# Kernel tuning notes

Measured on AMD Instinct MI355X. Metric: run time of the kernel, lower is better.

Reference implementation:

```python
import jax, jax.numpy as jnp
import numpy as np

B, S, H = 4, 2048, 1024
E, K, F = 8, 2, 4096


def setup_inputs() -> dict:
    key = jax.random.key(0)
    ks = jax.random.split(key, 6)
    x = jax.random.normal(ks[0], (B, S, H), dtype=jnp.float32)
    gate_w = jax.random.normal(ks[1], (H, E), dtype=jnp.float32) * 0.02
    w1 = jax.random.normal(ks[2], (E, H, F), dtype=jnp.float32) * 0.02
    b1 = jnp.zeros((E, F), dtype=jnp.float32)
    w2 = jax.random.normal(ks[3], (E, F, H), dtype=jnp.float32) * 0.02
    b2 = jnp.zeros((E, H), dtype=jnp.float32)
    return {"x": x, "gate_w": gate_w, "w1": w1, "b1": b1, "w2": w2, "b2": b2}


def reference(x, gate_w, w1, b1, w2, b2):
    # NOTE: the torch module masks expert inputs per token, but since each
    # expert's output is re-masked by the same mask, the math is exactly
    # out[t] = sum_i renorm_prob[t,i] * expert_{topk_idx[t,i]}(x[t]).
    # Dropout is identity in eval mode.
    T = B * S
    x_flat = x.reshape(T, H)

    gate_scores = x_flat @ gate_w                      # [T, E]
    gate_probs = jax.nn.softmax(gate_scores, axis=-1)  # [T, E]
    topk_vals, topk_idx = jax.lax.top_k(gate_probs, K)  # [T, K]
    topk_w = jax.nn.softmax(topk_vals, axis=-1)        # renormalize via softmax (as in source)

    # Combine weights per (token, expert): sum over top-k slots.
    onehot = jax.nn.one_hot(topk_idx, E, dtype=x.dtype)           # [T, K, E]
    comb = jnp.einsum('tk,tke->te', topk_w, onehot)               # [T, E]

    # Run all experts densely (faithful to naive module; combine masks out unrouted).
    h = jnp.einsum('th,ehf->etf', x_flat, w1) + b1[:, None, :]    # [E, T, F]
    h = jax.nn.relu(h)
    expert_out = jnp.einsum('etf,efh->eth', h, w2) + b2[:, None, :]  # [E, T, H]

    out_flat = jnp.einsum('te,eth->th', comb, expert_out)         # [T, H]
    output = out_flat.reshape(B, S, H)

    # Load-balance loss: KL(uniform || softmax(mean gate prob)), batchmean over E.
    expert_usage = gate_probs.mean(axis=0)                        # [E]
    log_sm = jax.nn.log_softmax(expert_usage, axis=0)
    uniform = jnp.full((E,), 1.0 / E, dtype=x.dtype)
    kl = jnp.sum(uniform * (jnp.log(uniform) - log_sm)) / E
    load_balance_loss = 0.01 * kl
    return output, load_balance_loss
```

## Files before the change

kernel.cpp:

```cpp
#include <hip/hip_runtime.h>
#include <stdint.h>

#define T_TOK 8192
#define HD 1024
#define NE 8
#define FD 4096
#define RALLOC 18432
#define G1 1152
#define G2 384
#define NKT1 16
#define GATE_BLOCKS 1024

typedef __attribute__((ext_vector_type(8))) short bf16x8;
typedef __attribute__((ext_vector_type(4))) float f32x4;
typedef __attribute__((ext_vector_type(4))) short s16x4;

__device__ __forceinline__ unsigned short f2bf(float f) {
  unsigned u = __builtin_bit_cast(unsigned, f);
  u += 0x7fffu + ((u >> 16) & 1u);
  return (unsigned short)(u >> 16);
}

__device__ __forceinline__ void gld_lds16(const void* g, void* l) {
  __builtin_amdgcn_global_load_lds(
      (const __attribute__((address_space(1))) void*)g,
      (__attribute__((address_space(3))) void*)l, 16, 0, 0);
}

__global__ __launch_bounds__(256) void k_transpose2(const float* __restrict__ w1,
                                                    const float* __restrict__ w2,
                                                    unsigned short* __restrict__ w1t,
                                                    unsigned short* __restrict__ w2t) {
  __shared__ unsigned short tile[64 * 80];
  const int i = blockIdx.x;
  const float* src;
  unsigned short* dst;
  int R, C, r0, c0;
  if (i < 8192) {
    const int e = i >> 10, rem = i & 1023;
    R = HD; C = FD; r0 = (rem >> 6) << 6; c0 = (rem & 63) << 6;
    src = w1 + (size_t)e * R * C; dst = w1t + (size_t)e * R * C;
  } else {
    const int e = (i - 8192) >> 10, rem = (i - 8192) & 1023;
    R = FD; C = HD; r0 = (rem >> 4) << 6; c0 = (rem & 15) << 6;
    src = w2 + (size_t)e * R * C; dst = w2t + (size_t)e * R * C;
  }
  const int tid = threadIdx.x;
  {
    const int r = tid >> 2, cg = (tid & 3) * 16;
    #pragma unroll
    for (int m = 0; m < 4; ++m) {
      float4 v = *(const float4*)(src + (size_t)(r0 + r) * C + c0 + cg + 4 * m);
      s16x4 pv;
      pv[0] = (short)f2bf(v.x); pv[1] = (short)f2bf(v.y);
      pv[2] = (short)f2bf(v.z); pv[3] = (short)f2bf(v.w);
      *(s16x4*)&tile[r * 80 + cg + 4 * m] = pv;
    }
  }
  __syncthreads();
  {
    const int c = tid >> 2, rg = (tid & 3) * 16;
    bf16x8 v0, v1;
    #pragma unroll
    for (int j = 0; j < 8; ++j) v0[j] = (short)tile[(rg + j) * 80 + c];
    #pragma unroll
    for (int j = 0; j < 8; ++j) v1[j] = (short)tile[(rg + 8 + j) * 80 + c];
    unsigned short* dp = dst + (size_t)(c0 + c) * R + r0 + rg;
    *(bf16x8*)dp = v0;
    *(bf16x8*)(dp + 8) = v1;
  }
}

__global__ __launch_bounds__(512) void k_gating(const float* __restrict__ x,
                                                const float* __restrict__ gw,
                                                int* __restrict__ toke,
                                                float* __restrict__ tokw,
                                                int* __restrict__ counts8,
                                                double* __restrict__ part,
                                                unsigned short* __restrict__ xbf) {
  __shared__ float gwT[8 * 1024];
  __shared__ double sp[8][8];
  __shared__ int scnt[8];
  const int tid = threadIdx.x;
  const int lane = tid & 63;
  const int w = tid >> 6;
  if (tid < 8) scnt[tid] = 0;
  #pragma unroll
  for (int rep = 0; rep < 16; ++rep) {
    int idx = rep * 512 + tid;
    gwT[(idx & 7) * 1024 + (idx >> 3)] = gw[idx];
  }
  __syncthreads();

  const int t = blockIdx.x * 8 + w;
  double acc[8];
  #pragma unroll
  for (int e = 0; e < 8; ++e) acc[e] = 0.0;
  const float* xr = x + (size_t)t * HD;
  unsigned short* xbr = xbf + (size_t)t * HD;
  #pragma unroll
  for (int j = 0; j < 4; ++j) {
    const int hh = j * 256 + lane * 4;
    float4 xv = *(const float4*)(xr + hh);
    s16x4 pv;
    pv[0] = (short)f2bf(xv.x); pv[1] = (short)f2bf(xv.y);
    pv[2] = (short)f2bf(xv.z); pv[3] = (short)f2bf(xv.w);
    *(s16x4*)(xbr + hh) = pv;
    #pragma unroll
    for (int e = 0; e < 8; ++e) {
      float4 gv = *(const float4*)(gwT + e * 1024 + hh);
      acc[e] += (double)xv.x * (double)gv.x;
      acc[e] += (double)xv.y * (double)gv.y;
      acc[e] += (double)xv.z * (double)gv.z;
      acc[e] += (double)xv.w * (double)gv.w;
    }
  }
  for (int off = 32; off > 0; off >>= 1) {
    #pragma unroll
    for (int e = 0; e < 8; ++e) acc[e] += __shfl_xor(acc[e], off, 64);
  }
  double m = acc[0];
  #pragma unroll
  for (int e = 1; e < 8; ++e) m = fmax(m, acc[e]);
  double p[8], ssum = 0.0;
  #pragma unroll
  for (int e = 0; e < 8; ++e) { p[e] = exp(acc[e] - m); ssum += p[e]; }
  double inv = 1.0 / ssum;
  #pragma unroll
  for (int e = 0; e < 8; ++e) p[e] *= inv;
  int e0 = 0;
  #pragma unroll
  for (int e = 1; e < 8; ++e) if (p[e] > p[e0]) e0 = e;
  int e1 = (e0 == 0) ? 1 : 0;
  #pragma unroll
  for (int e = 0; e < 8; ++e) if (e != e0 && p[e] > p[e1]) e1 = e;
  if (lane == 0) {
    double z = exp(p[e1] - p[e0]);
    double w0 = 1.0 / (1.0 + z);
    toke[2 * t] = e0; toke[2 * t + 1] = e1;
    tokw[2 * t] = (float)w0; tokw[2 * t + 1] = (float)(z / (1.0 + z));
    atomicAdd(&scnt[e0], 1);
    atomicAdd(&scnt[e1], 1);
    #pragma unroll
    for (int e = 0; e < 8; ++e) sp[w][e] = p[e];
  }
  __syncthreads();
  if (tid < 8) {
    double s = 0.0;
    #pragma unroll
    for (int q = 0; q < 8; ++q) s += sp[q][tid];
    part[(size_t)blockIdx.x * 8 + tid] = s;
    counts8[(size_t)blockIdx.x * 8 + tid] = scnt[tid];
  }
}

__global__ __launch_bounds__(256) void k_scan(const int* __restrict__ counts8,
                                              int* __restrict__ offs,
                                              int* __restrict__ cursors,
                                              const double* __restrict__ part,
                                              float* __restrict__ loss_out,
                                              int* __restrict__ rowmap,
                                              float* __restrict__ roww) {
  __shared__ double su[8];
  __shared__ int soffs[9];
  __shared__ int scnt[8];
  const int tid = threadIdx.x;
  const int e = tid >> 5, sub = tid & 31;
  double s = 0.0;
  int c = 0;
  for (int b = sub; b < GATE_BLOCKS; b += 32) {
    s += part[(size_t)b * 8 + e];
    c += counts8[(size_t)b * 8 + e];
  }
  for (int off = 16; off > 0; off >>= 1) {
    s += __shfl_xor(s, off, 64);
    c += __shfl_xor(c, off, 64);
  }
  if (sub == 0) { su[e] = s; scnt[e] = c; }
  __syncthreads();
  if (tid == 0) {
    int o = 0;
    for (int i = 0; i < 8; ++i) {
      soffs[i] = o; offs[i] = o; cursors[i * 16] = o;
      o += ((scnt[i] + 255) >> 8) << 8;
    }
    soffs[8] = o; offs[8] = o;
    double u[8], mx = -1e300;
    for (int i = 0; i < 8; ++i) { u[i] = su[i] / 8192.0; mx = fmax(mx, u[i]); }
    double se = 0.0;
    for (int i = 0; i < 8; ++i) se += exp(u[i] - mx);
    double lse = mx + log(se);
    double kl = 0.0;
    const double lu = log(0.125);
    for (int i = 0; i < 8; ++i) kl += 0.125 * (lu - (u[i] - lse));
    kl /= 8.0;
    loss_out[0] = (float)(0.01 * kl);
  }
  __syncthreads();
  for (int i = 0; i < 8; ++i) {
    int s0 = soffs[i] + scnt[i];
    int en = soffs[i + 1];
    for (int k = s0 + tid; k < en; k += 256) { rowmap[k] = 2 * T_TOK; roww[k] = 0.f; }
  }
}

__global__ __launch_bounds__(256) void k_scatter(const int* __restrict__ toke,
                                                 const float* __restrict__ tokw,
                                                 int* __restrict__ cursors,
                                                 int* __restrict__ rowmap,
                                                 float* __restrict__ roww) {
  const int t = blockIdx.x * 256 + threadIdx.x;
  const int lane = threadIdx.x & 63;
  #pragma unroll
  for (int k = 0; k < 2; ++k) {
    int e = toke[2 * t + k];
    float wv = tokw[2 * t + k];
    for (int ex = 0; ex < 8; ++ex) {
      unsigned long long mask = __ballot(e == ex);
      if (e == ex) {
        int leader = __ffsll((unsigned long long)mask) - 1;
        int rank = __popcll(mask & ((1ull << lane) - 1ull));
        int base = 0;
        if (lane == leader) base = atomicAdd(&cursors[ex * 16], __popcll(mask));
        base = __shfl(base, leader, 64);
        rowmap[base + rank] = 2 * t + k;
        roww[base + rank] = wv;
      }
    }
  }
}

#define RDA(buf, mh) do { _Pragma("unroll") for (int m_ = 0; m_ < 4; ++m_) { \
  af[m_][0] = *(const bf16x8*)(lds + (buf) * 65536 + wmOff + (mh) * 8192 + aoff[m_][0]); \
  af[m_][1] = *(const bf16x8*)(lds + (buf) * 65536 + wmOff + (mh) * 8192 + aoff[m_][1]); } } while (0)

#define RDB(buf, nh, B) do { _Pragma("unroll") for (int nf_ = 0; nf_ < 2; ++nf_) { \
  B[nf_][0] = *(const bf16x8*)(lds + (buf) * 65536 + wnOff + (nh) * 4096 + boff[nf_][0]); \
  B[nf_][1] = *(const bf16x8*)(lds + (buf) * 65536 + wnOff + (nh) * 4096 + boff[nf_][1]); } } while (0)

#define MMA(mh, nh, B) do { _Pragma("unroll") for (int m_ = 0; m_ < 4; ++m_) \
  _Pragma("unroll") for (int nf_ = 0; nf_ < 2; ++nf_) \
  _Pragma("unroll") for (int kh_ = 0; kh_ < 2; ++kh_) \
    acc[(mh) * 4 + m_][(nh) * 2 + nf_] = __builtin_amdgcn_mfma_f32_16x16x32_bf16( \
        af[m_][kh_], B[nf_][kh_], acc[(mh) * 4 + m_][(nh) * 2 + nf_], 0, 0, 0); } while (0)

#define SYNC_PRE() do { __builtin_amdgcn_sched_barrier(0); __builtin_amdgcn_s_barrier(); \
  asm volatile("s_waitcnt lgkmcnt(0)" ::: "memory"); __builtin_amdgcn_sched_barrier(0); \
  __builtin_amdgcn_s_setprio(1); } while (0)

#define SYNC_POST() do { __builtin_amdgcn_s_setprio(0); __builtin_amdgcn_sched_barrier(0); \
  __builtin_amdgcn_s_barrier(); __builtin_amdgcn_sched_barrier(0); } while (0)

#define SYNC_POST_VM() do { __builtin_amdgcn_s_setprio(0); __builtin_amdgcn_sched_barrier(0); \
  asm volatile("s_waitcnt vmcnt(4)" ::: "memory"); __builtin_amdgcn_sched_barrier(0); \
  __builtin_amdgcn_s_barrier(); __builtin_amdgcn_sched_barrier(0); } while (0)

#define FRAG_OFFSETS256() \
  int aoff[4][2], boff[2][2]; \
  { \
    const int kg = (lane >> 4) << 4; \
    _Pragma("unroll") \
    for (int m = 0; m < 4; ++m) { \
      int r = m * 16 + (lane & 15); \
      _Pragma("unroll") \
      for (int kh = 0; kh < 2; ++kh) \
        aoff[m][kh] = r * 128 + ((kh * 64 + kg) ^ ((r & 7) << 4)); \
    } \
    _Pragma("unroll") \
    for (int nf = 0; nf < 2; ++nf) { \
      int r = (wn & 1) * 64 + nf * 16 + (lane & 15); \
      _Pragma("unroll") \
      for (int kh = 0; kh < 2; ++kh) \
        boff[nf][kh] = r * 128 + ((kh * 64 + kg) ^ ((r & 7) << 4)); \
    } \
  }

__global__ __launch_bounds__(512, 2) void k_gemm1(const unsigned short* __restrict__ xbf,
                                                  const unsigned short* __restrict__ w1t,
                                                  const float* __restrict__ b1,
                                                  const int* __restrict__ rowmap,
                                                  const int* __restrict__ offs,
                                                  unsigned short* __restrict__ hbuf) {
  __shared__ char lds[131072];
  const int id = blockIdx.x;
  const int xcd = id & 7, j = id >> 3;
  const int lrt = j >> 4, nb = j & 15;
  const int ntr = offs[8] >> 8;
  const int q = ntr >> 3, r8 = ntr & 7;
  const int cnt = q + (xcd < r8 ? 1 : 0);
  if (lrt >= cnt) return;
  const int start = (xcd < r8) ? xcd * (q + 1) : r8 * (q + 1) + (xcd - r8) * q;
  const int rt = start + lrt;
  const int row0 = rt * 256;
  int e = 0;
  #pragma unroll
  for (int i = 1; i < 8; ++i) if (row0 >= offs[i]) e = i;
  const int n0 = nb * 256;
  const int tid = threadIdx.x;
  const int lane = tid & 63;
  const int wid = tid >> 6;
  const int wm = wid >> 2, wn = wid & 3;

  const int rl = tid >> 3;
  const int cbs = ((tid & 7) << 4) ^ ((rl & 7) << 4);
  const char* pA[2][2];
  #pragma unroll
  for (int h = 0; h < 2; ++h)
    #pragma unroll
    for (int l = 0; l < 2; ++l) {
      int tok = rowmap[row0 + h * 128 + l * 64 + rl] >> 1;
      pA[h][l] = (const char*)xbf + (size_t)tok * 2048 + cbs;
    }
  const char* pB00 = (const char*)w1t + (size_t)e * ((size_t)FD * HD * 2) +
                     (size_t)(n0 + rl) * 2048 + cbs;
  const int stw = wid * 1024;

#define STA1(buf, h, kt) do { \
  gld_lds16(pA[h][0] + (size_t)(kt) * 128, lds + (buf) * 65536 + (h) * 16384 + stw); \
  gld_lds16(pA[h][1] + (size_t)(kt) * 128, lds + (buf) * 65536 + (h) * 16384 + 8192 + stw); } while (0)
#define STB1(buf, h, kt) do { \
  gld_lds16(pB00 + (size_t)(h) * 128 * 2048 + (size_t)(kt) * 128, \
            lds + (buf) * 65536 + 32768 + (h) * 16384 + stw); \
  gld_lds16(pB00 + ((size_t)(h) * 128 + 64) * 2048 + (size_t)(kt) * 128, \
            lds + (buf) * 65536 + 32768 + (h) * 16384 + 8192 + stw); } while (0)

  FRAG_OFFSETS256();
  const int wmOff = wm * 16384;
  const int wnOff = 32768 + (wn >> 1) * 16384;

  f32x4 acc[8][4];
  #pragma unroll
  for (int a = 0; a < 8; ++a)
    #pragma unroll
    for (int b = 0; b < 4; ++b) acc[a][b] = (f32x4){0.f, 0.f, 0.f, 0.f};
  bf16x8 af[4][2], b0r[2][2], b1r[2][2];

  STA1(0, 0, 0); STA1(0, 1, 0); STB1(0, 0, 0); STB1(0, 1, 0);
  STB1(1, 0, 1); STB1(1, 1, 1);
  asm volatile("s_waitcnt vmcnt(4)" ::: "memory");
  __builtin_amdgcn_sched_barrier(0);
  __builtin_amdgcn_s_barrier();
  __builtin_amdgcn_sched_barrier(0);

  #pragma unroll 1
  for (int i = 0; i < NKT1 / 2; ++i) {
    const int k1 = 2 * i + 1, k2 = 2 * i + 2, k3 = 2 * i + 3;
    RDA(0, 0); RDB(0, 0, b0r); STA1(1, 0, k1); SYNC_PRE(); MMA(0, 0, b0r); SYNC_POST();
    RDB(0, 1, b1r);            STA1(1, 1, k1); SYNC_PRE(); MMA(0, 1, b1r); SYNC_POST();
    RDA(0, 1);                 STB1(0, 0, k2); SYNC_PRE(); MMA(1, 1, b1r); SYNC_POST();
                               STB1(0, 1, k2); SYNC_PRE(); MMA(1, 0, b0r); SYNC_POST_VM();
    RDA(1, 0); RDB(1, 0, b0r); STA1(0, 0, k2); SYNC_PRE(); MMA(0, 0, b0r); SYNC_POST();
    RDB(1, 1, b1r);            STA1(0, 1, k2); SYNC_PRE(); MMA(0, 1, b1r); SYNC_POST();
    RDA(1, 1);                 STB1(1, 0, k3); SYNC_PRE(); MMA(1, 1, b1r); SYNC_POST();
                               STB1(1, 1, k3); SYNC_PRE(); MMA(1, 0, b0r); SYNC_POST_VM();
  }

  asm volatile("s_waitcnt vmcnt(0)" ::: "memory");
  __builtin_amdgcn_sched_barrier(0);
  __syncthreads();
  #pragma unroll
  for (int na = 0; na < 4; ++na) {
    int c = wn * 64 + (na >> 1) * 32 + (na & 1) * 16 + (lane & 15);
    float bias = b1[(size_t)e * FD + n0 + c];
    #pragma unroll
    for (int ma = 0; ma < 8; ++ma) {
      #pragma unroll
      for (int j2 = 0; j2 < 4; ++j2) {
        int r = wm * 128 + (ma >> 2) * 64 + (ma & 3) * 16 + ((lane >> 4) << 2) + j2;
        float v = fmaxf(acc[ma][na][j2] + bias, 0.f);
        *(unsigned short*)(lds + r * 512 + ((c * 2) ^ ((r & 7) << 4))) = f2bf(v);
      }
    }
  }
  __syncthreads();
  #pragma unroll
  for (int s = 0; s < 16; ++s) {
    int flat = s * 512 + tid;
    int r = flat >> 5, ch = flat & 31;
    bf16x8 v = *(const bf16x8*)(lds + r * 512 + ((ch * 16) ^ ((r & 7) << 4)));
    *(bf16x8*)((char*)hbuf + (size_t)(row0 + r) * 8192 + (size_t)n0 * 2 + ch * 16) = v;
  }
#undef STA1
#undef STB1
}

__global__ __launch_bounds__(512, 2) void k_gemm2(const unsigned short* __restrict__ hbuf,
                                                  const unsigned short* __restrict__ w2t,
                                                  const float* __restrict__ b2,
                                                  const int* __restrict__ rowmap,
                                                  const float* __restrict__ roww,
                                                  const int* __restrict__ offs,
                                                  float* __restrict__ out2,
                                                  float* __restrict__ psplit) {
  __shared__ char lds[131072];
  const int id = blockIdx.x;
  int bx, by, kt0, niter, jj = -1;
  if (id < 256) {
    const int sid = (id & 7) * 32 + (id >> 3);
    bx = sid & 3; by = sid >> 2;
    kt0 = 0; niter = 32;
  } else {
    const int jid = id - 256;
    const int q = (jid & 7) * 16 + (jid >> 3);
    const int t = 256 + (q >> 2);
    const int nT2 = (offs[8] >> 8) * 4;
    if (t >= nT2) return;
    bx = t & 3; by = t >> 2;
    kt0 = (q & 3) * 16; niter = 8;
    jj = q;
  }
  const int row0 = by * 256;
  int e = 0;
  #pragma unroll
  for (int i = 1; i < 8; ++i) if (row0 >= offs[i]) e = i;
  const int n0 = bx * 256;
  const int tid = threadIdx.x;
  const int lane = tid & 63;
  const int wid = tid >> 6;
  const int wm = wid >> 2, wn = wid & 3;

  const int rl = tid >> 3;
  const int cbs = ((tid & 7) << 4) ^ ((rl & 7) << 4);
  const char* pA00 = (const char*)hbuf + (size_t)(row0 + rl) * 8192 + cbs;
  const char* pB00 = (const char*)w2t + (size_t)e * ((size_t)HD * FD * 2) +
                     (size_t)(n0 + rl) * 8192 + cbs;
  const int stw = wid * 1024;

#define STA2(buf, h, kt) do { \
  gld_lds16(pA00 + (size_t)(h) * 128 * 8192 + (size_t)(kt) * 128, \
            lds + (buf) * 65536 + (h) * 16384 + stw); \
  gld_lds16(pA00 + ((size_t)(h) * 128 + 64) * 8192 + (size_t)(kt) * 128, \
            lds + (buf) * 65536 + (h) * 16384 + 8192 + stw); } while (0)
#define STB2(buf, h, kt) do { \
  gld_lds16(pB00 + (size_t)(h) * 128 * 8192 + (size_t)(kt) * 128, \
            lds + (buf) * 65536 + 32768 + (h) * 16384 + stw); \
  gld_lds16(pB00 + ((size_t)(h) * 128 + 64) * 8192 + (size_t)(kt) * 128, \
            lds + (buf) * 65536 + 32768 + (h) * 16384 + 8192 + stw); } while (0)

  FRAG_OFFSETS256();
  const int wmOff = wm * 16384;
  const int wnOff = 32768 + (wn >> 1) * 16384;

  f32x4 acc[8][4];
  #pragma unroll
  for (int a = 0; a < 8; ++a)
    #pragma unroll
    for (int b = 0; b < 4; ++b) acc[a][b] = (f32x4){0.f, 0.f, 0.f, 0.f};
  bf16x8 af[4][2], b0r[2][2], b1r[2][2];

  STA2(0, 0, kt0); STA2(0, 1, kt0); STB2(0, 0, kt0); STB2(0, 1, kt0);
  STB2(1, 0, kt0 + 1); STB2(1, 1, kt0 + 1);
  asm volatile("s_waitcnt vmcnt(4)" ::: "memory");
  __builtin_amdgcn_sched_barrier(0);
  __builtin_amdgcn_s_barrier();
  __builtin_amdgcn_sched_barrier(0);

  #pragma unroll 1
  for (int i = 0; i < niter; ++i) {
    const int k1 = kt0 + 2 * i + 1, k2 = kt0 + 2 * i + 2, k3 = kt0 + 2 * i + 3;
    RDA(0, 0); RDB(0, 0, b0r); STA2(1, 0, k1); SYNC_PRE(); MMA(0, 0, b0r); SYNC_POST();
    RDB(0, 1, b1r);            STA2(1, 1, k1); SYNC_PRE(); MMA(0, 1, b1r); SYNC_POST();
    RDA(0, 1);                 STB2(0, 0, k2); SYNC_PRE(); MMA(1, 1, b1r); SYNC_POST();
                               STB2(0, 1, k2); SYNC_PRE(); MMA(1, 0, b0r); SYNC_POST_VM();
    RDA(1, 0); RDB(1, 0, b0r); STA2(0, 0, k2); SYNC_PRE(); MMA(0, 0, b0r); SYNC_POST();
    RDB(1, 1, b1r);            STA2(0, 1, k2); SYNC_PRE(); MMA(0, 1, b1r); SYNC_POST();
    RDA(1, 1);                 STB2(1, 0, k3); SYNC_PRE(); MMA(1, 1, b1r); SYNC_POST();
                               STB2(1, 1, k3); SYNC_PRE(); MMA(1, 0, b0r); SYNC_POST_VM();
  }

  asm volatile("s_waitcnt vmcnt(0)" ::: "memory");
  __builtin_amdgcn_sched_barrier(0);
  if (jj < 0) {
    #pragma unroll
    for (int ma = 0; ma < 8; ++ma) {
      #pragma unroll
      for (int j2 = 0; j2 < 4; ++j2) {
        int r = wm * 128 + (ma >> 2) * 64 + (ma & 3) * 16 + ((lane >> 4) << 2) + j2;
        int rm = rowmap[row0 + r];
        float wr = roww[row0 + r];
        float* orow = out2 + (size_t)rm * 1024 + n0;
        #pragma unroll
        for (int na = 0; na < 4; ++na) {
          int c = wn * 64 + (na >> 1) * 32 + (na & 1) * 16 + (lane & 15);
          orow[c] = (acc[ma][na][j2] + b2[(size_t)e * HD + n0 + c]) * wr;
        }
      }
    }
  } else {
    float* ps = psplit + (size_t)jj * 65536;
    #pragma unroll
    for (int ma = 0; ma < 8; ++ma) {
      #pragma unroll
      for (int j2 = 0; j2 < 4; ++j2) {
        int r = wm * 128 + (ma >> 2) * 64 + (ma & 3) * 16 + ((lane >> 4) << 2) + j2;
        #pragma unroll
        for (int na = 0; na < 4; ++na) {
          int c = wn * 64 + (na >> 1) * 32 + (na & 1) * 16 + (lane & 15);
          ps[r * 256 + c] = acc[ma][na][j2];
        }
      }
    }
  }
#undef STA2
#undef STB2
}

__global__ __launch_bounds__(512) void k_fix2(const float* __restrict__ psplit,
                                              const int* __restrict__ offs,
                                              const float* __restrict__ b2,
                                              const int* __restrict__ rowmap,
                                              const float* __restrict__ roww,
                                              float* __restrict__ out2) {
  const int nT2 = (offs[8] >> 8) * 4;
  const int t = 256 + blockIdx.x;
  if (t >= nT2) return;
  const int by = t >> 2, bx = t & 3;
  const int row0 = by * 256, n0 = bx * 256;
  int e = 0;
  #pragma unroll
  for (int i = 1; i < 8; ++i) if (row0 >= offs[i]) e = i;
  const float* ps = psplit + (size_t)blockIdx.x * 4 * 65536;
  const int cg = (threadIdx.x & 63) * 4;
  const int r0t = threadIdx.x >> 6;
  float4 bb = *(const float4*)(b2 + (size_t)e * HD + n0 + cg);
  for (int rr = 0; rr < 32; ++rr) {
    int r = rr * 8 + r0t;
    int rm = rowmap[row0 + r];
    float wr = roww[row0 + r];
    float4 s0 = *(const float4*)(ps + 0 * 65536 + r * 256 + cg);
    float4 s1 = *(const float4*)(ps + 1 * 65536 + r * 256 + cg);
    float4 s2 = *(const float4*)(ps + 2 * 65536 + r * 256 + cg);
    float4 s3 = *(const float4*)(ps + 3 * 65536 + r * 256 + cg);
    float4 o;
    o.x = wr * (s0.x + s1.x + s2.x + s3.x + bb.x);
    o.y = wr * (s0.y + s1.y + s2.y + s3.y + bb.y);
    o.z = wr * (s0.z + s1.z + s2.z + s3.z + bb.z);
    o.w = wr * (s0.w + s1.w + s2.w + s3.w + bb.w);
    *(float4*)(out2 + (size_t)rm * 1024 + n0 + cg) = o;
  }
}

__global__ __launch_bounds__(256) void k_combine(const float* __restrict__ out2,
                                                 float* __restrict__ out) {
  const int t = blockIdx.x;
  const int i = threadIdx.x * 4;
  float4 a = *(const float4*)(out2 + (size_t)(2 * t) * 1024 + i);
  float4 b = *(const float4*)(out2 + (size_t)(2 * t + 1) * 1024 + i);
  float4 r;
  r.x = a.x + b.x; r.y = a.y + b.y; r.z = a.z + b.z; r.w = a.w + b.w;
  *(float4*)(out + (size_t)t * 1024 + i) = r;
}

extern "C" void kernel_launch(void* const* d_in, const int* in_sizes, int n_in,
                              void* d_out, int out_size, void* d_ws, size_t ws_size,
                              hipStream_t stream) {
  const float* x = (const float*)d_in[0];
  const float* gw = (const float*)d_in[1];
  const float* w1 = (const float*)d_in[2];
  const float* b1 = (const float*)d_in[3];
  const float* w2 = (const float*)d_in[4];
  const float* b2 = (const float*)d_in[5];
  float* out = (float*)d_out;

  char* ws = (char*)d_ws;
  size_t o = 0;
  unsigned short* w2t = (unsigned short*)(ws + o); o += (size_t)NE * HD * FD * 2;
  unsigned short* hbuf = (unsigned short*)(ws + o); o += (size_t)RALLOC * FD * 2;
  unsigned short* w1t = (unsigned short*)(ws + o);
  size_t w1t_off = o; o += (size_t)NE * FD * HD * 2;
  unsigned short* xbf = (unsigned short*)(ws + o); o += (size_t)T_TOK * HD * 2;
  int* rowmap = (int*)(ws + o); o += (size_t)RALLOC * 4;
  float* roww = (float*)(ws + o); o += (size_t)RALLOC * 4;
  int* toke = (int*)(ws + o); o += (size_t)T_TOK * 2 * 4;
  float* tokw = (float*)(ws + o); o += (size_t)T_TOK * 2 * 4;
  double* part = (double*)(ws + o); o += (size_t)GATE_BLOCKS * 8 * 8;
  int* counts8 = (int*)(ws + o); o += (size_t)GATE_BLOCKS * 8 * 4;
  int* ctrl = (int*)(ws + o); o += 1024;
  int* offs = ctrl;
  int* cursors = ctrl + 64;
  float* psplit = (float*)(ws + o); o += (size_t)128 * 65536 * 4;
  float* out2 = (float*)(ws + w1t_off);

  k_transpose2<<<16384, 256, 0, stream>>>(w1, w2, w1t, w2t);
  k_gating<<<GATE_BLOCKS, 512, 0, stream>>>(x, gw, toke, tokw, counts8, part, xbf);
  k_scan<<<1, 256, 0, stream>>>(counts8, offs, cursors, part, out + (size_t)T_TOK * HD,
                                rowmap, roww);
  k_scatter<<<T_TOK / 256, 256, 0, stream>>>(toke, tokw, cursors, rowmap, roww);
  k_gemm1<<<G1, 512, 0, stream>>>(xbf, w1t, b1, rowmap, offs, hbuf);
  k_gemm2<<<G2, 512, 0, stream>>>(hbuf, w2t, b2, rowmap, roww, offs, out2, psplit);
  k_fix2<<<32, 512, 0, stream>>>(psplit, offs, b2, rowmap, roww, out2);
  k_combine<<<T_TOK, 256, 0, stream>>>(out2, out);
}
```

Baseline: 471.1 us.

## Fuse weight transpose with gating into one launch, merge MMA sync phases

```diff
diff --git a/kernel.cpp b/kernel.cpp
--- a/kernel.cpp
+++ b/kernel.cpp
@@ -9,7 +9,7 @@
 #define G1 1152
 #define G2 384
 #define NKT1 16
-#define GATE_BLOCKS 1024
+#define GATE_BLOCKS 2048
 
 typedef __attribute__((ext_vector_type(8))) short bf16x8;
 typedef __attribute__((ext_vector_type(4))) float f32x4;
@@ -27,130 +27,132 @@
       (__attribute__((address_space(3))) void*)l, 16, 0, 0);
 }
 
-__global__ __launch_bounds__(256) void k_transpose2(const float* __restrict__ w1,
-                                                    const float* __restrict__ w2,
-                                                    unsigned short* __restrict__ w1t,
-                                                    unsigned short* __restrict__ w2t) {
-  __shared__ unsigned short tile[64 * 80];
+__global__ __launch_bounds__(256) void k_prep(const float* __restrict__ w1,
+                                              const float* __restrict__ w2,
+                                              unsigned short* __restrict__ w1t,
+                                              unsigned short* __restrict__ w2t,
+                                              const float* __restrict__ x,
+                                              const float* __restrict__ gw,
+                                              int* __restrict__ toke,
+                                              float* __restrict__ tokw,
+                                              int* __restrict__ counts8,
+                                              double* __restrict__ part,
+                                              unsigned short* __restrict__ xbf) {
+  __shared__ char smem[33056];
   const int i = blockIdx.x;
-  const float* src;
-  unsigned short* dst;
-  int R, C, r0, c0;
-  if (i < 8192) {
-    const int e = i >> 10, rem = i & 1023;
-    R = HD; C = FD; r0 = (rem >> 6) << 6; c0 = (rem & 63) << 6;
-    src = w1 + (size_t)e * R * C; dst = w1t + (size_t)e * R * C;
+  const int tid = threadIdx.x;
+  if (i < 16384) {
+    unsigned short* tile = (unsigned short*)smem;
+    const float* src;
+    unsigned short* dst;
+    int R, C, r0, c0;
+    if (i < 8192) {
+      const int e = i >> 10, rem = i & 1023;
+      R = HD; C = FD; r0 = (rem >> 6) << 6; c0 = (rem & 63) << 6;
+      src = w1 + (size_t)e * R * C; dst = w1t + (size_t)e * R * C;
+    } else {
+      const int e = (i - 8192) >> 10, rem = (i - 8192) & 1023;
+      R = FD; C = HD; r0 = (rem >> 4) << 6; c0 = (rem & 15) << 6;
+      src = w2 + (size_t)e * R * C; dst = w2t + (size_t)e * R * C;
+    }
+    {
+      const int r = tid >> 2, cg = (tid & 3) * 16;
+      #pragma unroll
+      for (int m = 0; m < 4; ++m) {
+        float4 v = *(const float4*)(src + (size_t)(r0 + r) * C + c0 + cg + 4 * m);
+        s16x4 pv;
+        pv[0] = (short)f2bf(v.x); pv[1] = (short)f2bf(v.y);
+        pv[2] = (short)f2bf(v.z); pv[3] = (short)f2bf(v.w);
+        *(s16x4*)&tile[r * 80 + cg + 4 * m] = pv;
+      }
+    }
+    __syncthreads();
+    {
+      const int c = tid >> 2, rg = (tid & 3) * 16;
+      bf16x8 v0, v1;
+      #pragma unroll
+      for (int j = 0; j < 8; ++j) v0[j] = (short)tile[(rg + j) * 80 + c];
+      #pragma unroll
+      for (int j = 0; j < 8; ++j) v1[j] = (short)tile[(rg + 8 + j) * 80 + c];
+      unsigned short* dp = dst + (size_t)(c0 + c) * R + r0 + rg;
+      *(bf16x8*)dp = v0;
+      *(bf16x8*)(dp + 8) = v1;
+    }
   } else {
-    const int e = (i - 8192) >> 10, rem = (i - 8192) & 1023;
-    R = FD; C = HD; r0 = (rem >> 4) << 6; c0 = (rem & 15) << 6;
-    src = w2 + (size_t)e * R * C; dst = w2t + (size_t)e * R * C;
-  }
-  const int tid = threadIdx.x;
-  {
-    const int r = tid >> 2, cg = (tid & 3) * 16;
-    #pragma unroll
-    for (int m = 0; m < 4; ++m) {
-      float4 v = *(const float4*)(src + (size_t)(r0 + r) * C + c0 + cg + 4 * m);
+    float* gwT = (float*)smem;
+    double (*sp)[8] = (double(*)[8])(smem + 32768);
+    int* scnt = (int*)(smem + 33024);
+    const int gb = i - 16384;
+    const int lane = tid & 63;
+    const int w = tid >> 6;
+    if (tid < 8) scnt[tid] = 0;
+    #pragma unroll
+    for (int rep = 0; rep < 32; ++rep) {
+      int idx = rep * 256 + tid;
+      gwT[(idx & 7) * 1024 + (idx >> 3)] = gw[idx];
+    }
+    __syncthreads();
+
+    const int t = gb * 4 + w;
+    double acc[8];
+    #pragma unroll
+    for (int e = 0; e < 8; ++e) acc[e] = 0.0;
+    const float* xr = x + (size_t)t * HD;
+    unsigned short* xbr = xbf + (size_t)t * HD;
+    #pragma unroll
+    for (int j = 0; j < 4; ++j) {
+      const int hh = j * 256 + lane * 4;
+      float4 xv = *(const float4*)(xr + hh);
       s16x4 pv;
-      pv[0] = (short)f2bf(v.x); pv[1] = (short)f2bf(v.y);
-      pv[2] = (short)f2bf(v.z); pv[3] = (short)f2bf(v.w);
-      *(s16x4*)&tile[r * 80 + cg + 4 * m] = pv;
-    }
-  }
-  __syncthreads();
-  {
-    const int c = tid >> 2, rg = (tid & 3) * 16;
-    bf16x8 v0, v1;
-    #pragma unroll
-    for (int j = 0; j < 8; ++j) v0[j] = (short)tile[(rg + j) * 80 + c];
-    #pragma unroll
-    for (int j = 0; j < 8; ++j) v1[j] = (short)tile[(rg + 8 + j) * 80 + c];
-    unsigned short* dp = dst + (size_t)(c0 + c) * R + r0 + rg;
-    *(bf16x8*)dp = v0;
-    *(bf16x8*)(dp + 8) = v1;
-  }
-}
-
-__global__ __launch_bounds__(512) void k_gating(const float* __restrict__ x,
-                                                const float* __restrict__ gw,
-                                                int* __restrict__ toke,
-                                                float* __restrict__ tokw,
-                                                int* __restrict__ counts8,
-                                                double* __restrict__ part,
-                                                unsigned short* __restrict__ xbf) {
-  __shared__ float gwT[8 * 1024];
-  __shared__ double sp[8][8];
-  __shared__ int scnt[8];
-  const int tid = threadIdx.x;
-  const int lane = tid & 63;
-  const int w = tid >> 6;
-  if (tid < 8) scnt[tid] = 0;
-  #pragma unroll
-  for (int rep = 0; rep < 16; ++rep) {
-    int idx = rep * 512 + tid;
-    gwT[(idx & 7) * 1024 + (idx >> 3)] = gw[idx];
-  }
-  __syncthreads();
-
-  const int t = blockIdx.x * 8 + w;
-  double acc[8];
-  #pragma unroll
-  for (int e = 0; e < 8; ++e) acc[e] = 0.0;
-  const float* xr = x + (size_t)t * HD;
-  unsigned short* xbr = xbf + (size_t)t * HD;
-  #pragma unroll
-  for (int j = 0; j < 4; ++j) {
-    const int hh = j * 256 + lane * 4;
-    float4 xv = *(const float4*)(xr + hh);
-    s16x4 pv;
-    pv[0] = (short)f2bf(xv.x); pv[1] = (short)f2bf(xv.y);
-    pv[2] = (short)f2bf(xv.z); pv[3] = (short)f2bf(xv.w);
-    *(s16x4*)(xbr + hh) = pv;
-    #pragma unroll
-    for (int e = 0; e < 8; ++e) {
-      float4 gv = *(const float4*)(gwT + e * 1024 + hh);
-      acc[e] += (double)xv.x * (double)gv.x;
-      acc[e] += (double)xv.y * (double)gv.y;
-      acc[e] += (double)xv.z * (double)gv.z;
-      acc[e] += (double)xv.w * (double)gv.w;
-    }
-  }
-  for (int off = 32; off > 0; off >>= 1) {
-    #pragma unroll
-    for (int e = 0; e < 8; ++e) acc[e] += __shfl_xor(acc[e], off, 64);
-  }
-  double m = acc[0];
-  #pragma unroll
-  for (int e = 1; e < 8; ++e) m = fmax(m, acc[e]);
-  double p[8], ssum = 0.0;
-  #pragma unroll
-  for (int e = 0; e < 8; ++e) { p[e] = exp(acc[e] - m); ssum += p[e]; }
-  double inv = 1.0 / ssum;
-  #pragma unroll
-  for (int e = 0; e < 8; ++e) p[e] *= inv;
-  int e0 = 0;
-  #pragma unroll
-  for (int e = 1; e < 8; ++e) if (p[e] > p[e0]) e0 = e;
-  int e1 = (e0 == 0) ? 1 : 0;
-  #pragma unroll
-  for (int e = 0; e < 8; ++e) if (e != e0 && p[e] > p[e1]) e1 = e;
-  if (lane == 0) {
-    double z = exp(p[e1] - p[e0]);
-    double w0 = 1.0 / (1.0 + z);
-    toke[2 * t] = e0; toke[2 * t + 1] = e1;
-    tokw[2 * t] = (float)w0; tokw[2 * t + 1] = (float)(z / (1.0 + z));
-    atomicAdd(&scnt[e0], 1);
-    atomicAdd(&scnt[e1], 1);
-    #pragma unroll
-    for (int e = 0; e < 8; ++e) sp[w][e] = p[e];
-  }
-  __syncthreads();
-  if (tid < 8) {
-    double s = 0.0;
-    #pragma unroll
-    for (int q = 0; q < 8; ++q) s += sp[q][tid];
-    part[(size_t)blockIdx.x * 8 + tid] = s;
-    counts8[(size_t)blockIdx.x * 8 + tid] = scnt[tid];
+      pv[0] = (short)f2bf(xv.x); pv[1] = (short)f2bf(xv.y);
+      pv[2] = (short)f2bf(xv.z); pv[3] = (short)f2bf(xv.w);
+      *(s16x4*)(xbr + hh) = pv;
+      #pragma unroll
+      for (int e = 0; e < 8; ++e) {
+        float4 gv = *(const float4*)(gwT + e * 1024 + hh);
+        acc[e] += (double)xv.x * (double)gv.x;
+        acc[e] += (double)xv.y * (double)gv.y;
+        acc[e] += (double)xv.z * (double)gv.z;
+        acc[e] += (double)xv.w * (double)gv.w;
+      }
+    }
+    for (int off = 32; off > 0; off >>= 1) {
+      #pragma unroll
+      for (int e = 0; e < 8; ++e) acc[e] += __shfl_xor(acc[e], off, 64);
+    }
+    double m = acc[0];
+    #pragma unroll
+    for (int e = 1; e < 8; ++e) m = fmax(m, acc[e]);
+    double p[8], ssum = 0.0;
+    #pragma unroll
+    for (int e = 0; e < 8; ++e) { p[e] = exp(acc[e] - m); ssum += p[e]; }
+    double inv = 1.0 / ssum;
+    #pragma unroll
+    for (int e = 0; e < 8; ++e) p[e] *= inv;
+    int e0 = 0;
+    #pragma unroll
+    for (int e = 1; e < 8; ++e) if (p[e] > p[e0]) e0 = e;
+    int e1 = (e0 == 0) ? 1 : 0;
+    #pragma unroll
+    for (int e = 0; e < 8; ++e) if (e != e0 && p[e] > p[e1]) e1 = e;
+    if (lane == 0) {
+      double z = exp(p[e1] - p[e0]);
+      double w0 = 1.0 / (1.0 + z);
+      toke[2 * t] = e0; toke[2 * t + 1] = e1;
+      tokw[2 * t] = (float)w0; tokw[2 * t + 1] = (float)(z / (1.0 + z));
+      atomicAdd(&scnt[e0], 1);
+      atomicAdd(&scnt[e1], 1);
+      #pragma unroll
+      for (int e = 0; e < 8; ++e) sp[w][e] = p[e];
+    }
+    __syncthreads();
+    if (tid < 8) {
+      double s = 0.0;
+      #pragma unroll
+      for (int q = 0; q < 4; ++q) s += sp[q][tid];
+      part[(size_t)gb * 8 + tid] = s;
+      counts8[(size_t)gb * 8 + tid] = scnt[tid];
+    }
   }
 }
 
@@ -345,14 +347,14 @@
   #pragma unroll 1
   for (int i = 0; i < NKT1 / 2; ++i) {
     const int k1 = 2 * i + 1, k2 = 2 * i + 2, k3 = 2 * i + 3;
-    RDA(0, 0); RDB(0, 0, b0r); STA1(1, 0, k1); SYNC_PRE(); MMA(0, 0, b0r); SYNC_POST();
-    RDB(0, 1, b1r);            STA1(1, 1, k1); SYNC_PRE(); MMA(0, 1, b1r); SYNC_POST();
-    RDA(0, 1);                 STB1(0, 0, k2); SYNC_PRE(); MMA(1, 1, b1r); SYNC_POST();
-                               STB1(0, 1, k2); SYNC_PRE(); MMA(1, 0, b0r); SYNC_POST_VM();
-    RDA(1, 0); RDB(1, 0, b0r); STA1(0, 0, k2); SYNC_PRE(); MMA(0, 0, b0r); SYNC_POST();
-    RDB(1, 1, b1r);            STA1(0, 1, k2); SYNC_PRE(); MMA(0, 1, b1r); SYNC_POST();
-    RDA(1, 1);                 STB1(1, 0, k3); SYNC_PRE(); MMA(1, 1, b1r); SYNC_POST();
-                               STB1(1, 1, k3); SYNC_PRE(); MMA(1, 0, b0r); SYNC_POST_VM();
+    RDA(0, 0); RDB(0, 0, b0r); RDB(0, 1, b1r); STA1(1, 0, k1); STA1(1, 1, k1);
+      SYNC_PRE(); MMA(0, 0, b0r); MMA(0, 1, b1r); SYNC_POST();
+    RDA(0, 1); STB1(0, 0, k2); STB1(0, 1, k2);
+      SYNC_PRE(); MMA(1, 0, b0r); MMA(1, 1, b1r); SYNC_POST_VM();
+    RDA(1, 0); RDB(1, 0, b0r); RDB(1, 1, b1r); STA1(0, 0, k2); STA1(0, 1, k2);
+      SYNC_PRE(); MMA(0, 0, b0r); MMA(0, 1, b1r); SYNC_POST();
+    RDA(1, 1); STB1(1, 0, k3); STB1(1, 1, k3);
+      SYNC_PRE(); MMA(1, 0, b0r); MMA(1, 1, b1r); SYNC_POST_VM();
   }
 
   asm volatile("s_waitcnt vmcnt(0)" ::: "memory");
@@ -458,14 +460,14 @@
   #pragma unroll 1
   for (int i = 0; i < niter; ++i) {
     const int k1 = kt0 + 2 * i + 1, k2 = kt0 + 2 * i + 2, k3 = kt0 + 2 * i + 3;
-    RDA(0, 0); RDB(0, 0, b0r); STA2(1, 0, k1); SYNC_PRE(); MMA(0, 0, b0r); SYNC_POST();
-    RDB(0, 1, b1r);            STA2(1, 1, k1); SYNC_PRE(); MMA(0, 1, b1r); SYNC_POST();
-    RDA(0, 1);                 STB2(0, 0, k2); SYNC_PRE(); MMA(1, 1, b1r); SYNC_POST();
-                               STB2(0, 1, k2); SYNC_PRE(); MMA(1, 0, b0r); SYNC_POST_VM();
-    RDA(1, 0); RDB(1, 0, b0r); STA2(0, 0, k2); SYNC_PRE(); MMA(0, 0, b0r); SYNC_POST();
-    RDB(1, 1, b1r);            STA2(0, 1, k2); SYNC_PRE(); MMA(0, 1, b1r); SYNC_POST();
-    RDA(1, 1);                 STB2(1, 0, k3); SYNC_PRE(); MMA(1, 1, b1r); SYNC_POST();
-                               STB2(1, 1, k3); SYNC_PRE(); MMA(1, 0, b0r); SYNC_POST_VM();
+    RDA(0, 0); RDB(0, 0, b0r); RDB(0, 1, b1r); STA2(1, 0, k1); STA2(1, 1, k1);
+      SYNC_PRE(); MMA(0, 0, b0r); MMA(0, 1, b1r); SYNC_POST();
+    RDA(0, 1); STB2(0, 0, k2); STB2(0, 1, k2);
+      SYNC_PRE(); MMA(1, 0, b0r); MMA(1, 1, b1r); SYNC_POST_VM();
+    RDA(1, 0); RDB(1, 0, b0r); RDB(1, 1, b1r); STA2(0, 0, k2); STA2(0, 1, k2);
+      SYNC_PRE(); MMA(0, 0, b0r); MMA(0, 1, b1r); SYNC_POST();
+    RDA(1, 1); STB2(1, 0, k3); STB2(1, 1, k3);
+      SYNC_PRE(); MMA(1, 0, b0r); MMA(1, 1, b1r); SYNC_POST_VM();
   }
 
   asm volatile("s_waitcnt vmcnt(0)" ::: "memory");
@@ -581,8 +583,8 @@
   float* psplit = (float*)(ws + o); o += (size_t)128 * 65536 * 4;
   float* out2 = (float*)(ws + w1t_off);
 
-  k_transpose2<<<16384, 256, 0, stream>>>(w1, w2, w1t, w2t);
-  k_gating<<<GATE_BLOCKS, 512, 0, stream>>>(x, gw, toke, tokw, counts8, part, xbf);
+  k_prep<<<16384 + GATE_BLOCKS, 256, 0, stream>>>(w1, w2, w1t, w2t, x, gw, toke, tokw,
+                                                  counts8, part, xbf);
   k_scan<<<1, 256, 0, stream>>>(counts8, offs, cursors, part, out + (size_t)T_TOK * HD,
                                 rowmap, roww);
   k_scatter<<<T_TOK / 256, 256, 0, stream>>>(toke, tokw, cursors, rowmap, roww);
```

Measured after the change: 478.2 us. Within noise of the previous version (+1.5%).
